# Kernel tuning notes

Hardware: AMD Instinct MI355X
Metric: run time of the kernel (lower is better)

The kernel has to match this reference:

```python
import jax, jax.numpy as jnp
import numpy as np

N = 50000
E = 800000
G_DIM = 128
HEADS = 8
DEPTH = 3
EPS = 1e-5


def _ln(x, w, b):
    m = jnp.mean(x, axis=-1, keepdims=True)
    v = jnp.var(x, axis=-1, keepdims=True)
    return (x - m) * jax.lax.rsqrt(v + EPS) * w + b


def setup_inputs() -> dict:
    key = jax.random.key(0)
    ks = jax.random.split(key, 12)
    s = 0.02
    inp = {
        "h": jax.random.normal(ks[0], (N, G_DIM), jnp.float32),
        "src": jax.random.randint(ks[1], (E,), 0, N, jnp.int32),
        "dst": jax.random.randint(ks[2], (E,), 0, N, jnp.int32),
        # outer norm
        "norm_w": jnp.ones((G_DIM,), jnp.float32),
        "norm_b": jnp.zeros((G_DIM,), jnp.float32),
        # attention norm_in
        "nin_w": jnp.ones((G_DIM,), jnp.float32),
        "nin_b": jnp.zeros((G_DIM,), jnp.float32),
        # to_qkv (no bias)
        "Wqkv": jax.random.normal(ks[3], (G_DIM, 3 * G_DIM), jnp.float32) * s,
        # ff norm_out
        "no_w": jnp.ones((G_DIM,), jnp.float32),
        "no_b": jnp.zeros((G_DIM,), jnp.float32),
        # ff linears (hidden = 4*g_dim)
        "W1": jax.random.normal(ks[4], (G_DIM, 4 * G_DIM), jnp.float32) * s,
        "b1": jnp.zeros((4 * G_DIM,), jnp.float32),
        "W2": jax.random.normal(ks[5], (4 * G_DIM, G_DIM), jnp.float32) * s,
        "b2": jnp.zeros((G_DIM,), jnp.float32),
    }
    return inp


def _graph_attention(x, src, dst, nin_w, nin_b, Wqkv):
    # x: [N, g_dim]
    s = _ln(x, nin_w, nin_b)
    qkv = s @ Wqkv                                   # [N, 3*g_dim]
    q, k, v = jnp.split(qkv, 3, axis=-1)
    D = G_DIM // HEADS
    q = q.reshape(N, HEADS, D)
    k = k.reshape(N, HEADS, D)
    v = v.reshape(N, HEADS, D)
    scale = G_DIM ** (-0.5)
    # edge scores: elementwise q[src] * k[dst] per (head, dim) channel
    att = q[src] * k[dst] * scale                    # [E, H, D]
    # edge softmax over incoming edges of each dst node, per channel
    mx = jax.ops.segment_max(att, dst, num_segments=N)   # [N, H, D]
    e = jnp.exp(att - mx[dst])
    z = jax.ops.segment_sum(e, dst, num_segments=N)      # [N, H, D]
    a = e / z[dst]
    # weighted message aggregation
    rst = jax.ops.segment_sum(v[src] * a, dst, num_segments=N)  # [N, H, D]
    return rst.reshape(N, G_DIM)


def reference(h, src, dst, norm_w, norm_b, nin_w, nin_b, Wqkv,
              no_w, no_b, W1, b1, W2, b2):
    for _ in range(DEPTH):
        x = _ln(h, norm_w, norm_b)
        x = _graph_attention(x, src, dst, nin_w, nin_b, Wqkv)
        # feedforward with its own pre-norm
        y = _ln(x, no_w, no_b)
        y = jax.nn.gelu(y @ W1 + b1, approximate=False) @ W2 + b2
        h = y + h
    return h
```

## Files before the change

kernel.cpp:

```cpp
#include <hip/hip_runtime.h>
#include <math.h>

#define N_NODES 50000
#define N_EDGES 800000
#define EPS 1e-5f

#define SCAN_CHUNK 1024
#define SCAN_NBLK ((N_NODES + SCAN_CHUNK - 1) / SCAN_CHUNK)

typedef unsigned short u16;
typedef __attribute__((ext_vector_type(8))) u16 u16x8;
typedef __attribute__((ext_vector_type(8))) short bf16x8;
typedef __attribute__((ext_vector_type(4))) float f32x4;

__device__ __forceinline__ u16 f2bf(float x) {
  unsigned u = __float_as_uint(x);
  return (u16)((u + 0x7FFFu + ((u >> 16) & 1u)) >> 16);
}
__device__ __forceinline__ float bf2f(u16 b) {
  return __uint_as_float(((unsigned)b) << 16);
}

__device__ __forceinline__ void async_ld16(u16* lds, const u16* g) {
  __builtin_amdgcn_global_load_lds(
      (const __attribute__((address_space(1))) unsigned int*)g,
      (__attribute__((address_space(3))) unsigned int*)lds, 16, 0, 0);
}

__global__ void count_kernel(const int* __restrict__ dst, int* __restrict__ cnt, int e_total) {
  int e = blockIdx.x * 256 + threadIdx.x;
  if (e < e_total) atomicAdd(&cnt[dst[e]], 1);
}

__global__ __launch_bounds__(256) void scan1_kernel(const int* __restrict__ cnt,
                                                    int* __restrict__ offs,
                                                    int* __restrict__ bsum, int n) {
  __shared__ int buf[256];
  int t = threadIdx.x;
  int base = blockIdx.x * SCAN_CHUNK + t * 4;
  int v0 = (base + 0 < n) ? cnt[base + 0] : 0;
  int v1 = (base + 1 < n) ? cnt[base + 1] : 0;
  int v2 = (base + 2 < n) ? cnt[base + 2] : 0;
  int v3 = (base + 3 < n) ? cnt[base + 3] : 0;
  int tsum = v0 + v1 + v2 + v3;
  buf[t] = tsum;
  __syncthreads();
  for (int st = 1; st < 256; st <<= 1) {
    int x = (t >= st) ? buf[t - st] : 0;
    __syncthreads();
    buf[t] += x;
    __syncthreads();
  }
  int texcl = buf[t] - tsum;
  if (base + 0 < n) offs[base + 0] = texcl;
  if (base + 1 < n) offs[base + 1] = texcl + v0;
  if (base + 2 < n) offs[base + 2] = texcl + v0 + v1;
  if (base + 3 < n) offs[base + 3] = texcl + v0 + v1 + v2;
  if (t == 255) bsum[blockIdx.x] = buf[255];
}

__global__ void scan2_kernel(const int* __restrict__ bsum, int* __restrict__ bbase) {
  int lane = threadIdx.x;
  int v = (lane < SCAN_NBLK) ? bsum[lane] : 0;
  int orig = v;
#pragma unroll
  for (int ofs = 1; ofs < 64; ofs <<= 1) {
    int u = __shfl_up(v, ofs, 64);
    if (lane >= ofs) v += u;
  }
  if (lane < SCAN_NBLK) bbase[lane] = v - orig;
}

__global__ __launch_bounds__(256) void scan3_kernel(int* __restrict__ offs,
                                                    int* __restrict__ cursor,
                                                    const int* __restrict__ bbase, int n) {
  int t = threadIdx.x;
  int b = bbase[blockIdx.x];
  int base = blockIdx.x * SCAN_CHUNK + t * 4;
#pragma unroll
  for (int j = 0; j < 4; ++j) {
    int i = base + j;
    if (i < n) {
      int o = offs[i] + b;
      offs[i] = o;
      cursor[i] = o;
    }
  }
  if (blockIdx.x == 0 && t == 0) offs[n] = N_EDGES;
}

__global__ void scatter_kernel(const int* __restrict__ src, const int* __restrict__ dst,
                               int* __restrict__ cursor, int* __restrict__ ssrc, int e_total) {
  int e = blockIdx.x * 256 + threadIdx.x;
  if (e < e_total) {
    int p = atomicAdd(&cursor[dst[e]], 1);
    ssrc[p] = src[e];
  }
}

__global__ void wsplit_kernel(const float* __restrict__ W, u16* __restrict__ outH,
                              u16* __restrict__ outL, int K, int M) {
  int e = blockIdx.x * 256 + threadIdx.x;
  if (e >= K * M) return;
  int n = e % M, k = e / M;
  float a = W[e];
  u16 hb = f2bf(a);
  outH[(size_t)n * K + k] = hb;
  outL[(size_t)n * K + k] = f2bf(a - bf2f(hb));
}

__device__ __forceinline__ float wave_sum(float v) {
#pragma unroll
  for (int m = 32; m > 0; m >>= 1) v += __shfl_xor(v, m, 64);
  return v;
}

__global__ __launch_bounds__(256) void ln2_kernel(
    const float* __restrict__ h,
    const float* __restrict__ w1, const float* __restrict__ b1,
    const float* __restrict__ w2, const float* __restrict__ b2,
    u16* __restrict__ s_hi, u16* __restrict__ s_lo, int n) {
  int lane = threadIdx.x & 63;
  int row = blockIdx.x * 4 + (threadIdx.x >> 6);
  if (row >= n) return;
  float2 v = ((const float2*)(h + (size_t)row * 128))[lane];
  float s = wave_sum(v.x + v.y);
  float q = wave_sum(v.x * v.x + v.y * v.y);
  float mean = s * (1.0f / 128.0f);
  float var = q * (1.0f / 128.0f) - mean * mean;
  float rs = 1.0f / sqrtf(var + EPS);
  float2 wv = ((const float2*)w1)[lane];
  float2 bv = ((const float2*)b1)[lane];
  float x0 = (v.x - mean) * rs * wv.x + bv.x;
  float x1 = (v.y - mean) * rs * wv.y + bv.y;
  float s2 = wave_sum(x0 + x1);
  float q2 = wave_sum(x0 * x0 + x1 * x1);
  float mean2 = s2 * (1.0f / 128.0f);
  float var2 = q2 * (1.0f / 128.0f) - mean2 * mean2;
  float rs2 = 1.0f / sqrtf(var2 + EPS);
  float2 wv2 = ((const float2*)w2)[lane];
  float2 bv2 = ((const float2*)b2)[lane];
  float o0 = (x0 - mean2) * rs2 * wv2.x + bv2.x;
  float o1 = (x1 - mean2) * rs2 * wv2.y + bv2.y;
  u16 h0 = f2bf(o0), h1 = f2bf(o1);
  u16 l0 = f2bf(o0 - bf2f(h0)), l1 = f2bf(o1 - bf2f(h1));
  ((unsigned*)s_hi)[(size_t)row * 64 + lane] = (unsigned)h0 | ((unsigned)h1 << 16);
  ((unsigned*)s_lo)[(size_t)row * 64 + lane] = (unsigned)l0 | ((unsigned)l1 << 16);
}

__global__ __launch_bounds__(256) void ln1_kernel(
    const float* __restrict__ h,
    const float* __restrict__ w1, const float* __restrict__ b1,
    u16* __restrict__ s_hi, u16* __restrict__ s_lo, int n) {
  int lane = threadIdx.x & 63;
  int row = blockIdx.x * 4 + (threadIdx.x >> 6);
  if (row >= n) return;
  float2 v = ((const float2*)(h + (size_t)row * 128))[lane];
  float s = wave_sum(v.x + v.y);
  float q = wave_sum(v.x * v.x + v.y * v.y);
  float mean = s * (1.0f / 128.0f);
  float var = q * (1.0f / 128.0f) - mean * mean;
  float rs = 1.0f / sqrtf(var + EPS);
  float2 wv = ((const float2*)w1)[lane];
  float2 bv = ((const float2*)b1)[lane];
  float o0 = (v.x - mean) * rs * wv.x + bv.x;
  float o1 = (v.y - mean) * rs * wv.y + bv.y;
  u16 h0 = f2bf(o0), h1 = f2bf(o1);
  u16 l0 = f2bf(o0 - bf2f(h0)), l1 = f2bf(o1 - bf2f(h1));
  ((unsigned*)s_hi)[(size_t)row * 64 + lane] = (unsigned)h0 | ((unsigned)h1 << 16);
  ((unsigned*)s_lo)[(size_t)row * 64 + lane] = (unsigned)l0 | ((unsigned)l1 << 16);
}

__global__ __launch_bounds__(256) void attn_kernel(
    const u16* __restrict__ qv, const float* __restrict__ kbuf,
    const int* __restrict__ offs, const int* __restrict__ ssrc,
    float* __restrict__ rst, int n) {
  int lane = threadIdx.x & 63;
  int node = blockIdx.x * 4 + (threadIdx.x >> 6);
  if (node >= n) return;
  const float SCALE = 0.08838834764831845f;
  float2 kc = ((const float2*)(kbuf + (size_t)node * 128))[lane];
  kc.x *= SCALE; kc.y *= SCALE;
  int e0 = offs[node], e1 = offs[node + 1];
  float z0 = 0.f, z1 = 0.f, a0 = 0.f, a1 = 0.f;
  int e = e0;
  for (; e + 1 < e1; e += 2) {
    int s0 = ssrc[e], s1 = ssrc[e + 1];
    ushort4 wa = ((const ushort4*)(qv + (size_t)s0 * 256))[lane];
    ushort4 wb = ((const ushort4*)(qv + (size_t)s1 * 256))[lane];
    float pa0 = __expf(bf2f(wa.x) * kc.x), pa1 = __expf(bf2f(wa.y) * kc.y);
    float pb0 = __expf(bf2f(wb.x) * kc.x), pb1 = __expf(bf2f(wb.y) * kc.y);
    z0 += pa0 + pb0;
    z1 += pa1 + pb1;
    a0 = fmaf(pa0, bf2f(wa.z), fmaf(pb0, bf2f(wb.z), a0));
    a1 = fmaf(pa1, bf2f(wa.w), fmaf(pb1, bf2f(wb.w), a1));
  }
  if (e < e1) {
    int s0 = ssrc[e];
    ushort4 wa = ((const ushort4*)(qv + (size_t)s0 * 256))[lane];
    float pa0 = __expf(bf2f(wa.x) * kc.x), pa1 = __expf(bf2f(wa.y) * kc.y);
    z0 += pa0; z1 += pa1;
    a0 = fmaf(pa0, bf2f(wa.z), a0);
    a1 = fmaf(pa1, bf2f(wa.w), a1);
  }
  float2 o;
  o.x = (e1 > e0) ? a0 / z0 : 0.f;
  o.y = (e1 > e0) ? a1 / z1 : 0.f;
  ((float2*)(rst + (size_t)node * 128))[lane] = o;
}

template <int ACT, bool SPLITA, int K>
__global__ __launch_bounds__(256) void gemm_split(
    const u16* __restrict__ Ah, const u16* __restrict__ Al,
    const u16* __restrict__ BhT, const u16* __restrict__ BlT,
    const float* __restrict__ bias, const float* __restrict__ res,
    float* __restrict__ outF, u16* __restrict__ outH,
    u16* __restrict__ qvb, float* __restrict__ kbuf,
    int nrows, int M) {
  extern __shared__ u16 smem[];
  constexpr int PLANE = 4096;
  constexpr int SBUF = (SPLITA ? 4 : 3) * PLANE;
  constexpr int NT = K / 32;
  int tid = threadIdx.x;
  int lane = tid & 63;
  int wid = tid >> 6;
  int wr = wid >> 1, wc = wid & 1;
  int lr = lane & 15, lg = lane >> 4;
  int row0 = blockIdx.y * 128, col0 = blockIdx.x * 128;
  bool full_tile = (row0 + 128 <= nrows);
  int kb8 = lg * 8;

  f32x4 acc[4][4] = {};

  auto stage = [&](int buf, int k0) {
    u16* base = smem + buf * SBUF;
#pragma unroll
    for (int i = 0; i < 2; ++i) {
      int sub = wid * 2 + i;
      int arow = min(row0 + sub * 16 + lr, nrows - 1);
      int bcol = col0 + sub * 16 + lr;
      async_ld16(base + sub * 512, Ah + (size_t)arow * K + k0 + kb8);
      async_ld16(base + PLANE + sub * 512, BhT + (size_t)bcol * K + k0 + kb8);
      async_ld16(base + 2 * PLANE + sub * 512, BlT + (size_t)bcol * K + k0 + kb8);
      if (SPLITA)
        async_ld16(base + 3 * PLANE + sub * 512, Al + (size_t)arow * K + k0 + kb8);
    }
  };

  stage(0, 0);
  __syncthreads();

#pragma unroll 2
  for (int t = 0; t < NT; ++t) {
    int cur = t & 1;
    if (t + 1 < NT) stage(cur ^ 1, (t + 1) * 32);
    const u16* base = smem + cur * SBUF;
    bf16x8 afh[4], afl[4], bfh[4], bfl[4];
#pragma unroll
    for (int mi = 0; mi < 4; ++mi) {
      afh[mi] = *(const bf16x8*)(base + (wr * 4 + mi) * 512 + lane * 8);
      if (SPLITA) afl[mi] = *(const bf16x8*)(base + 3 * PLANE + (wr * 4 + mi) * 512 + lane * 8);
    }
#pragma unroll
    for (int ni = 0; ni < 4; ++ni) {
      bfh[ni] = *(const bf16x8*)(base + PLANE + (wc * 4 + ni) * 512 + lane * 8);
      bfl[ni] = *(const bf16x8*)(base + 2 * PLANE + (wc * 4 + ni) * 512 + lane * 8);
    }
#pragma unroll
    for (int mi = 0; mi < 4; ++mi)
#pragma unroll
      for (int ni = 0; ni < 4; ++ni) {
        acc[mi][ni] = __builtin_amdgcn_mfma_f32_16x16x32_bf16(afh[mi], bfh[ni], acc[mi][ni], 0, 0, 0);
        if (SPLITA)
          acc[mi][ni] = __builtin_amdgcn_mfma_f32_16x16x32_bf16(afl[mi], bfh[ni], acc[mi][ni], 0, 0, 0);
        acc[mi][ni] = __builtin_amdgcn_mfma_f32_16x16x32_bf16(afh[mi], bfl[ni], acc[mi][ni], 0, 0, 0);
      }
    __syncthreads();
  }

#pragma unroll
  for (int mi = 0; mi < 4; ++mi) {
#pragma unroll
    for (int j = 0; j < 4; ++j) {
      int r = row0 + wr * 64 + mi * 16 + lg * 4 + j;
      if (!full_tile && r >= nrows) continue;
#pragma unroll
      for (int ni = 0; ni < 4; ++ni) {
        int c = col0 + wc * 64 + ni * 16 + lr;
        float v = acc[mi][ni][j];
        if (ACT == 0) {
          if (c < 128) {
            qvb[(size_t)r * 256 + ((c >> 1) << 2) + (c & 1)] = f2bf(v);
          } else if (c < 256) {
            kbuf[(size_t)r * 128 + (c - 128)] = v;
          } else {
            int cc = c - 256;
            qvb[(size_t)r * 256 + ((cc >> 1) << 2) + 2 + (cc & 1)] = f2bf(v);
          }
        } else if (ACT == 1) {
          v += bias[c];
          v = 0.5f * v * (1.0f + erff(v * 0.70710678118654752f));
          outH[(size_t)r * M + c] = f2bf(v);
        } else {
          v += bias[c] + res[(size_t)r * M + c];
          outF[(size_t)r * M + c] = v;
        }
      }
    }
  }
}

extern "C" void kernel_launch(void* const* d_in, const int* in_sizes, int n_in,
                              void* d_out, int out_size, void* d_ws, size_t ws_size,
                              hipStream_t stream) {
  const float* h_in   = (const float*)d_in[0];
  const int*   src    = (const int*)d_in[1];
  const int*   dst    = (const int*)d_in[2];
  const float* norm_w = (const float*)d_in[3];
  const float* norm_b = (const float*)d_in[4];
  const float* nin_w  = (const float*)d_in[5];
  const float* nin_b  = (const float*)d_in[6];
  const float* Wqkv   = (const float*)d_in[7];
  const float* no_w   = (const float*)d_in[8];
  const float* no_b   = (const float*)d_in[9];
  const float* W1     = (const float*)d_in[10];
  const float* b1     = (const float*)d_in[11];
  const float* W2     = (const float*)d_in[12];
  const float* b2     = (const float*)d_in[13];
  float* out = (float*)d_out;

  char* wsp = (char*)d_ws;
  float* h_cur = (float*)wsp;             wsp += (size_t)N_NODES * 128 * 4;
  u16* s_hi = (u16*)wsp;                  wsp += (size_t)N_NODES * 128 * 2;
  u16* s_lo = (u16*)wsp;                  wsp += (size_t)N_NODES * 128 * 2;
  u16* qvb  = (u16*)wsp;                  wsp += (size_t)N_NODES * 256 * 2;
  float* kbuf = (float*)wsp;              wsp += (size_t)N_NODES * 128 * 4;
  u16* hid  = (u16*)wsp;                  wsp += (size_t)N_NODES * 512 * 2;
  u16* WqT_h = (u16*)wsp; wsp += 49152 * 2;
  u16* WqT_l = (u16*)wsp; wsp += 49152 * 2;
  u16* W1T_h = (u16*)wsp; wsp += 65536 * 2;
  u16* W1T_l = (u16*)wsp; wsp += 65536 * 2;
  u16* W2T_h = (u16*)wsp; wsp += 65536 * 2;
  u16* W2T_l = (u16*)wsp; wsp += 65536 * 2;
  int* cnt    = (int*)wsp;
  int* cursor = cnt + N_NODES;
  int* offs   = cursor + N_NODES;
  int* ssrc   = offs + N_NODES + 1;
  int* bsum   = ssrc + N_EDGES;
  int* bbase  = bsum + 64;

  hipMemsetAsync(cnt, 0, N_NODES * sizeof(int), stream);
  count_kernel<<<(N_EDGES + 255) / 256, 256, 0, stream>>>(dst, cnt, N_EDGES);
  scan1_kernel<<<SCAN_NBLK, 256, 0, stream>>>(cnt, offs, bsum, N_NODES);
  scan2_kernel<<<1, 64, 0, stream>>>(bsum, bbase);
  scan3_kernel<<<SCAN_NBLK, 256, 0, stream>>>(offs, cursor, bbase, N_NODES);
  scatter_kernel<<<(N_EDGES + 255) / 256, 256, 0, stream>>>(src, dst, cursor, ssrc, N_EDGES);

  wsplit_kernel<<<(128 * 384 + 255) / 256, 256, 0, stream>>>(Wqkv, WqT_h, WqT_l, 128, 384);
  wsplit_kernel<<<(128 * 512 + 255) / 256, 256, 0, stream>>>(W1, W1T_h, W1T_l, 128, 512);
  wsplit_kernel<<<(512 * 128 + 255) / 256, 256, 0, stream>>>(W2, W2T_h, W2T_l, 512, 128);

  const int grid_rows = (N_NODES + 127) / 128;
  constexpr size_t SH_SPLIT = 2u * 4 * 4096 * 2;
  constexpr size_t SH_NOSPLIT = 2u * 3 * 4096 * 2;

  for (int layer = 0; layer < 3; ++layer) {
    const float* h_src = (layer == 0) ? h_in : h_cur;
    float* h_dst = (layer == 2) ? out : h_cur;

    ln2_kernel<<<12500, 256, 0, stream>>>(h_src, norm_w, norm_b, nin_w, nin_b, s_hi, s_lo, N_NODES);
    gemm_split<0, true, 128><<<dim3(3, grid_rows), 256, SH_SPLIT, stream>>>(
        s_hi, s_lo, WqT_h, WqT_l, nullptr, nullptr,
        nullptr, nullptr, qvb, kbuf, N_NODES, 384);
    attn_kernel<<<12500, 256, 0, stream>>>(qvb, kbuf, offs, ssrc, out, N_NODES);
    ln1_kernel<<<12500, 256, 0, stream>>>(out, no_w, no_b, s_hi, s_lo, N_NODES);
    gemm_split<1, true, 128><<<dim3(4, grid_rows), 256, SH_SPLIT, stream>>>(
        s_hi, s_lo, W1T_h, W1T_l, b1, nullptr,
        nullptr, hid, nullptr, nullptr, N_NODES, 512);
    gemm_split<2, false, 512><<<dim3(1, grid_rows), 256, SH_NOSPLIT, stream>>>(
        hid, nullptr, W2T_h, W2T_l, b2, h_src,
        h_dst, nullptr, nullptr, nullptr, N_NODES, 128);
  }
}
```

Measured before the change: 918.0 us.

## Keep B tile resident in LDS and stream A fragments directly from global

```diff
diff --git a/kernel.cpp b/kernel.cpp
--- a/kernel.cpp
+++ b/kernel.cpp
@@ -9,7 +9,6 @@
 #define SCAN_NBLK ((N_NODES + SCAN_CHUNK - 1) / SCAN_CHUNK)
 
 typedef unsigned short u16;
-typedef __attribute__((ext_vector_type(8))) u16 u16x8;
 typedef __attribute__((ext_vector_type(8))) short bf16x8;
 typedef __attribute__((ext_vector_type(4))) float f32x4;
 
@@ -209,8 +208,8 @@
   ((float2*)(rst + (size_t)node * 128))[lane] = o;
 }
 
-template <int ACT, bool SPLITA, int K>
-__global__ __launch_bounds__(256) void gemm_split(
+template <int ACT, bool SPLITA, int K, int NI, int WR, int WC>
+__global__ __launch_bounds__(256) void gemm_bstat(
     const u16* __restrict__ Ah, const u16* __restrict__ Al,
     const u16* __restrict__ BhT, const u16* __restrict__ BlT,
     const float* __restrict__ bias, const float* __restrict__ res,
@@ -218,75 +217,91 @@
     u16* __restrict__ qvb, float* __restrict__ kbuf,
     int nrows, int M) {
   extern __shared__ u16 smem[];
-  constexpr int PLANE = 4096;
-  constexpr int SBUF = (SPLITA ? 4 : 3) * PLANE;
-  constexpr int NT = K / 32;
+  constexpr int BCOLS = WC * NI * 16;
+  constexpr int NKT = K / 32;
+  constexpr int NSUB = BCOLS / 16;
+  constexpr int BCK = BCOLS * K;
   int tid = threadIdx.x;
   int lane = tid & 63;
   int wid = tid >> 6;
-  int wr = wid >> 1, wc = wid & 1;
+  int wr = wid / WC, wc = wid % WC;
   int lr = lane & 15, lg = lane >> 4;
-  int row0 = blockIdx.y * 128, col0 = blockIdx.x * 128;
-  bool full_tile = (row0 + 128 <= nrows);
-  int kb8 = lg * 8;
-
-  f32x4 acc[4][4] = {};
-
-  auto stage = [&](int buf, int k0) {
-    u16* base = smem + buf * SBUF;
-#pragma unroll
-    for (int i = 0; i < 2; ++i) {
-      int sub = wid * 2 + i;
-      int arow = min(row0 + sub * 16 + lr, nrows - 1);
-      int bcol = col0 + sub * 16 + lr;
-      async_ld16(base + sub * 512, Ah + (size_t)arow * K + k0 + kb8);
-      async_ld16(base + PLANE + sub * 512, BhT + (size_t)bcol * K + k0 + kb8);
-      async_ld16(base + 2 * PLANE + sub * 512, BlT + (size_t)bcol * K + k0 + kb8);
-      if (SPLITA)
-        async_ld16(base + 3 * PLANE + sub * 512, Al + (size_t)arow * K + k0 + kb8);
-    }
+  int row0 = blockIdx.y * (WR * 64);
+  int col0 = blockIdx.x * BCOLS;
+  bool full_tile = (row0 + WR * 64 <= nrows);
+
+  constexpr int NJOB = NSUB * NKT * 2;
+#pragma unroll
+  for (int jj = 0; jj < NJOB / 4; ++jj) {
+    int j = jj * 4 + wid;
+    int p = j / (NSUB * NKT);
+    int r = j % (NSUB * NKT);
+    int sub = r / NKT, kt = r % NKT;
+    const u16* srcb = p ? BlT : BhT;
+    async_ld16(smem + p * BCK + r * 512,
+               srcb + (size_t)(col0 + sub * 16 + lr) * K + kt * 32 + lg * 8);
+  }
+  __syncthreads();
+
+  f32x4 acc[4][NI] = {};
+  int wrow0 = row0 + wr * 64;
+  int nclamp = nrows - 1;
+
+  auto aload = [&](const u16* __restrict__ A, int mi, int kt) -> bf16x8 {
+    int rrow = min(wrow0 + mi * 16 + lr, nclamp);
+    return *(const bf16x8*)(A + (size_t)rrow * K + kt * 32 + lg * 8);
   };
 
-  stage(0, 0);
-  __syncthreads();
-
-#pragma unroll 2
-  for (int t = 0; t < NT; ++t) {
-    int cur = t & 1;
-    if (t + 1 < NT) stage(cur ^ 1, (t + 1) * 32);
-    const u16* base = smem + cur * SBUF;
-    bf16x8 afh[4], afl[4], bfh[4], bfl[4];
-#pragma unroll
-    for (int mi = 0; mi < 4; ++mi) {
-      afh[mi] = *(const bf16x8*)(base + (wr * 4 + mi) * 512 + lane * 8);
-      if (SPLITA) afl[mi] = *(const bf16x8*)(base + 3 * PLANE + (wr * 4 + mi) * 512 + lane * 8);
-    }
-#pragma unroll
-    for (int ni = 0; ni < 4; ++ni) {
-      bfh[ni] = *(const bf16x8*)(base + PLANE + (wc * 4 + ni) * 512 + lane * 8);
-      bfl[ni] = *(const bf16x8*)(base + 2 * PLANE + (wc * 4 + ni) * 512 + lane * 8);
+  bf16x8 ah_c[4], al_c[4], ah_n[4], al_n[4];
+#pragma unroll
+  for (int mi = 0; mi < 4; ++mi) {
+    ah_c[mi] = aload(Ah, mi, 0);
+    if (SPLITA) al_c[mi] = aload(Al, mi, 0);
+  }
+
+#pragma unroll
+  for (int kt = 0; kt < NKT; ++kt) {
+    if (kt + 1 < NKT) {
+#pragma unroll
+      for (int mi = 0; mi < 4; ++mi) {
+        ah_n[mi] = aload(Ah, mi, kt + 1);
+        if (SPLITA) al_n[mi] = aload(Al, mi, kt + 1);
+      }
+    }
+    bf16x8 bh[NI], bl[NI];
+#pragma unroll
+    for (int ni = 0; ni < NI; ++ni) {
+      const u16* bp = smem + ((wc * NI + ni) * NKT + kt) * 512 + lane * 8;
+      bh[ni] = *(const bf16x8*)bp;
+      bl[ni] = *(const bf16x8*)(bp + BCK);
     }
 #pragma unroll
     for (int mi = 0; mi < 4; ++mi)
 #pragma unroll
-      for (int ni = 0; ni < 4; ++ni) {
-        acc[mi][ni] = __builtin_amdgcn_mfma_f32_16x16x32_bf16(afh[mi], bfh[ni], acc[mi][ni], 0, 0, 0);
+      for (int ni = 0; ni < NI; ++ni) {
+        acc[mi][ni] = __builtin_amdgcn_mfma_f32_16x16x32_bf16(ah_c[mi], bh[ni], acc[mi][ni], 0, 0, 0);
         if (SPLITA)
-          acc[mi][ni] = __builtin_amdgcn_mfma_f32_16x16x32_bf16(afl[mi], bfh[ni], acc[mi][ni], 0, 0, 0);
-        acc[mi][ni] = __builtin_amdgcn_mfma_f32_16x16x32_bf16(afh[mi], bfl[ni], acc[mi][ni], 0, 0, 0);
+          acc[mi][ni] = __builtin_amdgcn_mfma_f32_16x16x32_bf16(al_c[mi], bh[ni], acc[mi][ni], 0, 0, 0);
+        acc[mi][ni] = __builtin_amdgcn_mfma_f32_16x16x32_bf16(ah_c[mi], bl[ni], acc[mi][ni], 0, 0, 0);
       }
-    __syncthreads();
+    if (kt + 1 < NKT) {
+#pragma unroll
+      for (int mi = 0; mi < 4; ++mi) {
+        ah_c[mi] = ah_n[mi];
+        if (SPLITA) al_c[mi] = al_n[mi];
+      }
+    }
   }
 
 #pragma unroll
   for (int mi = 0; mi < 4; ++mi) {
 #pragma unroll
     for (int j = 0; j < 4; ++j) {
-      int r = row0 + wr * 64 + mi * 16 + lg * 4 + j;
+      int r = wrow0 + mi * 16 + lg * 4 + j;
       if (!full_tile && r >= nrows) continue;
 #pragma unroll
-      for (int ni = 0; ni < 4; ++ni) {
-        int c = col0 + wc * 64 + ni * 16 + lr;
+      for (int ni = 0; ni < NI; ++ni) {
+        int c = col0 + wc * NI * 16 + ni * 16 + lr;
         float v = acc[mi][ni][j];
         if (ACT == 0) {
           if (c < 128) {
@@ -360,24 +375,24 @@
   wsplit_kernel<<<(128 * 512 + 255) / 256, 256, 0, stream>>>(W1, W1T_h, W1T_l, 128, 512);
   wsplit_kernel<<<(512 * 128 + 255) / 256, 256, 0, stream>>>(W2, W2T_h, W2T_l, 512, 128);
 
-  const int grid_rows = (N_NODES + 127) / 128;
-  constexpr size_t SH_SPLIT = 2u * 4 * 4096 * 2;
-  constexpr size_t SH_NOSPLIT = 2u * 3 * 4096 * 2;
+  const int gr128 = (N_NODES + 127) / 128;
+  const int gr256 = (N_NODES + 255) / 256;
+  constexpr size_t SH = 65536;
 
   for (int layer = 0; layer < 3; ++layer) {
     const float* h_src = (layer == 0) ? h_in : h_cur;
     float* h_dst = (layer == 2) ? out : h_cur;
 
     ln2_kernel<<<12500, 256, 0, stream>>>(h_src, norm_w, norm_b, nin_w, nin_b, s_hi, s_lo, N_NODES);
-    gemm_split<0, true, 128><<<dim3(3, grid_rows), 256, SH_SPLIT, stream>>>(
+    gemm_bstat<0, true, 128, 4, 2, 2><<<dim3(3, gr128), 256, SH, stream>>>(
         s_hi, s_lo, WqT_h, WqT_l, nullptr, nullptr,
         nullptr, nullptr, qvb, kbuf, N_NODES, 384);
     attn_kernel<<<12500, 256, 0, stream>>>(qvb, kbuf, offs, ssrc, out, N_NODES);
     ln1_kernel<<<12500, 256, 0, stream>>>(out, no_w, no_b, s_hi, s_lo, N_NODES);
-    gemm_split<1, true, 128><<<dim3(4, grid_rows), 256, SH_SPLIT, stream>>>(
+    gemm_bstat<1, true, 128, 4, 2, 2><<<dim3(4, gr128), 256, SH, stream>>>(
         s_hi, s_lo, W1T_h, W1T_l, b1, nullptr,
         nullptr, hid, nullptr, nullptr, N_NODES, 512);
-    gemm_split<2, false, 512><<<dim3(1, grid_rows), 256, SH_NOSPLIT, stream>>>(
+    gemm_bstat<2, false, 512, 2, 4, 1><<<dim3(4, gr256), 256, SH, stream>>>(
         hid, nullptr, W2T_h, W2T_l, b2, h_src,
         h_dst, nullptr, nullptr, nullptr, N_NODES, 128);
   }
```

Measured after the change: 1.050 ms. 1.14x slower.
